# Performance work log

Measured on AMD Instinct MI355X. Metric: run time of the kernel, lower is better.

## Reference

```python
import jax, jax.numpy as jnp
import numpy as np

N_EMBD = 2048
N_EXPERTS = 8
MOE_LOSS_COEFF = 0.01


def setup_inputs() -> dict:
    key = jax.random.key(0)
    kx, kw = jax.random.split(key)
    x = jax.random.normal(kx, (4, 4096, N_EMBD), dtype=jnp.float32)
    # nn.Linear(n_embd, n_experts, bias=False): weight [n_experts, n_embd]
    bound = 1.0 / np.sqrt(N_EMBD)
    W = jax.random.uniform(kw, (N_EXPERTS, N_EMBD), dtype=jnp.float32,
                           minval=-bound, maxval=bound)
    return {"x": x, "W": W}


def reference(x, W):
    n_experts = W.shape[0]
    # gate linear: logits [B, T, E]
    logits = jnp.einsum("btd,ed->bte", x, W)
    probs = jax.nn.softmax(logits, axis=-1)
    # top-2 selection and renormalization
    top2_vals, top2_idx = jax.lax.top_k(probs, 2)  # [B,T,2]
    gate_probs_top2 = top2_vals / jnp.sum(top2_vals, axis=-1, keepdims=True)
    # aux load-balancing loss stats
    importance = jnp.mean(probs, axis=(0, 1))  # [E]
    top1_idx = jnp.argmax(probs, axis=-1)      # [B,T]
    one_hot = jax.nn.one_hot(top1_idx, n_experts, dtype=jnp.float32)
    load = jnp.mean(one_hot, axis=(0, 1))      # [E]
    aux_loss = n_experts * jnp.sum(importance * load) * MOE_LOSS_COEFF
    return gate_probs_top2, top2_idx, aux_loss
```

## Files before the change

### kernel.cpp

```cpp
#include <hip/hip_runtime.h>

#define NEMBD 2048
#define ROW4 (NEMBD / 4)
#define CHUNKS (ROW4 / 64)

__global__ __launch_bounds__(256) void gate_kernel(
    const float* __restrict__ x, const float* __restrict__ W,
    float* __restrict__ out, float* __restrict__ ws, int ntok)
{
    const int tid  = threadIdx.x;
    const int lane = tid & 63;
    const int wid  = tid >> 6;

    const int t0 = blockIdx.x * 8 + wid * 2;
    const bool va0 = t0 < ntok, va1 = (t0 + 1) < ntok;

    const float4* X4 = (const float4*)x;
    const float4* W4 = (const float4*)W;
    float* out_p = out;
    float* out_i = out + 2 * ntok;

    float a[16];
    #pragma unroll
    for (int q = 0; q < 16; ++q) a[q] = 0.f;

    const float4 z4 = make_float4(0.f, 0.f, 0.f, 0.f);

    #pragma unroll 2
    for (int i = 0; i < CHUNKS; ++i) {
        const int col = i * 64 + lane;
        float4 x0 = va0 ? X4[(size_t)t0 * ROW4 + col] : z4;
        float4 x1 = va1 ? X4[(size_t)(t0 + 1) * ROW4 + col] : z4;
        #pragma unroll
        for (int e = 0; e < 8; ++e) {
            float4 wv = W4[e * ROW4 + col];
            a[e]     += x0.x * wv.x + x0.y * wv.y + x0.z * wv.z + x0.w * wv.w;
            a[8 + e] += x1.x * wv.x + x1.y * wv.y + x1.z * wv.z + x1.w * wv.w;
        }
    }

    #pragma unroll
    for (int q = 0; q < 16; ++q) a[q] += __shfl_xor(a[q], 32, 64);
    #pragma unroll
    for (int q = 0; q < 16; ++q) a[q] += __shfl_xor(a[q], 16, 64);
    #pragma unroll
    for (int s = 0; s < 4; ++s) {
        const int hm = 8 >> s;
        const bool hi = (lane & hm) != 0;
        #pragma unroll
        for (int q = 0; q < 8; ++q) {
            if (q < hm) {
                float send = hi ? a[q] : a[q + hm];
                float recv = __shfl_xor(send, hm, 64);
                float keep = hi ? a[q + hm] : a[q];
                a[q] = keep + recv;
            }
        }
    }
    const float logit = a[0];
    const int e = lane & 7;
    const int k = (lane >> 3) & 1;
    const bool tvalid = (t0 + k) < ntok;

    float m = logit;
    #pragma unroll
    for (int mm = 1; mm <= 4; mm <<= 1) m = fmaxf(m, __shfl_xor(m, mm, 64));
    float p = __expf(logit - m);
    float ssum = p;
    #pragma unroll
    for (int mm = 1; mm <= 4; mm <<= 1) ssum += __shfl_xor(ssum, mm, 64);
    const float prob = p / ssum;

    float v1 = prob, v2 = -1.f;
    int   i1 = e,    i2 = -1;
    #pragma unroll
    for (int mm = 1; mm <= 4; mm <<= 1) {
        float b1 = __shfl_xor(v1, mm, 64);
        float b2 = __shfl_xor(v2, mm, 64);
        int  bi1 = __shfl_xor(i1, mm, 64);
        int  bi2 = __shfl_xor(i2, mm, 64);
        bool aw = (v1 > b1) || (v1 == b1 && i1 < bi1);
        float w1 = aw ? v1 : b1;  int wi1 = aw ? i1 : bi1;
        float l1 = aw ? b1 : v1;  int li1 = aw ? bi1 : i1;
        float w2 = aw ? v2 : b2;  int wi2 = aw ? i2 : bi2;
        bool sw = (l1 > w2) || (l1 == w2 && li1 < wi2);
        v1 = w1; i1 = wi1;
        v2 = sw ? l1 : w2;  i2 = sw ? li1 : wi2;
    }

    if (e == 0 && lane < 16 && tvalid) {
        const int t = t0 + k;
        const float denom = v1 + v2;
        out_p[2 * t]     = v1 / denom;
        out_p[2 * t + 1] = v2 / denom;
        out_i[2 * t]     = (float)i1;
        out_i[2 * t + 1] = (float)i2;
    }

    float pc = tvalid ? prob : 0.f;
    float oc = (tvalid && e == i1) ? 1.f : 0.f;
    pc += __shfl_xor(pc, 8, 64);
    oc += __shfl_xor(oc, 8, 64);

    __shared__ float part[4][16];
    if (lane < 8) {
        part[wid][lane]     = pc;
        part[wid][lane + 8] = oc;
    }
    __syncthreads();
    if (tid < 16) {
        atomicAdd(&ws[tid],
                  part[0][tid] + part[1][tid] + part[2][tid] + part[3][tid]);
    }
}

__global__ void finalize_kernel(const float* __restrict__ ws,
                                float* __restrict__ out, int ntok)
{
    if (threadIdx.x == 0) {
        const float inv = 1.f / (float)ntok;
        float aux = 0.f;
        #pragma unroll
        for (int e = 0; e < 8; ++e)
            aux += (ws[e] * inv) * (ws[8 + e] * inv);
        out[4 * ntok] = 8.f * aux * 0.01f;
    }
}

extern "C" void kernel_launch(void* const* d_in, const int* in_sizes, int n_in,
                              void* d_out, int out_size, void* d_ws, size_t ws_size,
                              hipStream_t stream)
{
    const float* x = (const float*)d_in[0];
    const float* W = (const float*)d_in[1];
    const int ntok    = in_sizes[0] / NEMBD;
    const int nblocks = (ntok + 7) / 8;

    hipMemsetAsync(d_ws, 0, 16 * sizeof(float), stream);
    gate_kernel<<<nblocks, 256, 0, stream>>>(
        x, W, (float*)d_out, (float*)d_ws, ntok);
    finalize_kernel<<<1, 64, 0, stream>>>(
        (const float*)d_ws, (float*)d_out, ntok);
}
```

Baseline: 215.0 us.

## Stage gate weights in LDS with 1024-thread blocks and per-block partial stats

Result: no change. 211.4 us (-1.7%).

```diff
diff --git a/kernel.cpp b/kernel.cpp
--- a/kernel.cpp
+++ b/kernel.cpp
@@ -3,20 +3,30 @@
 #define NEMBD 2048
 #define ROW4 (NEMBD / 4)
 #define CHUNKS (ROW4 / 64)
+#define NEXP 8
+#define W4N (NEXP * ROW4)
 
-__global__ __launch_bounds__(256) void gate_kernel(
+__global__ __launch_bounds__(1024) void gate_kernel(
     const float* __restrict__ x, const float* __restrict__ W,
     float* __restrict__ out, float* __restrict__ ws, int ntok)
 {
+    __shared__ float4 Wl[W4N];
+
     const int tid  = threadIdx.x;
     const int lane = tid & 63;
     const int wid  = tid >> 6;
 
-    const int t0 = blockIdx.x * 8 + wid * 2;
+    const float4* X4 = (const float4*)x;
+    const float4* W4 = (const float4*)W;
+
+    #pragma unroll
+    for (int k = 0; k < 4; ++k)
+        Wl[tid + k * 1024] = W4[tid + k * 1024];
+    __syncthreads();
+
+    const int t0 = blockIdx.x * 32 + wid * 2;
     const bool va0 = t0 < ntok, va1 = (t0 + 1) < ntok;
 
-    const float4* X4 = (const float4*)x;
-    const float4* W4 = (const float4*)W;
     float* out_p = out;
     float* out_i = out + 2 * ntok;
 
@@ -33,7 +43,7 @@
         float4 x1 = va1 ? X4[(size_t)(t0 + 1) * ROW4 + col] : z4;
         #pragma unroll
         for (int e = 0; e < 8; ++e) {
-            float4 wv = W4[e * ROW4 + col];
+            float4 wv = Wl[e * ROW4 + col];
             a[e]     += x0.x * wv.x + x0.y * wv.y + x0.z * wv.z + x0.w * wv.w;
             a[8 + e] += x1.x * wv.x + x1.y * wv.y + x1.z * wv.z + x1.w * wv.w;
         }
@@ -102,27 +112,43 @@
     pc += __shfl_xor(pc, 8, 64);
     oc += __shfl_xor(oc, 8, 64);
 
-    __shared__ float part[4][16];
-    if (lane < 8) {
-        part[wid][lane]     = pc;
-        part[wid][lane + 8] = oc;
-    }
+    float* part = (float*)Wl;
+    __syncthreads();
+    if (lane < 8)       part[wid * 16 + lane] = pc;
+    else if (lane < 16) part[wid * 16 + lane] = oc;
     __syncthreads();
     if (tid < 16) {
-        atomicAdd(&ws[tid],
-                  part[0][tid] + part[1][tid] + part[2][tid] + part[3][tid]);
+        float v = 0.f;
+        #pragma unroll
+        for (int w = 0; w < 16; ++w) v += part[w * 16 + tid];
+        ws[blockIdx.x * 16 + tid] = v;
     }
 }
 
 __global__ void finalize_kernel(const float* __restrict__ ws,
-                                float* __restrict__ out, int ntok)
+                                float* __restrict__ out, int nblk, int ntok)
 {
-    if (threadIdx.x == 0) {
+    __shared__ float s[16][16];
+    __shared__ float tot[16];
+    const int t = threadIdx.x;
+    const int slot = t & 15, chunk = t >> 4;
+    float p = 0.f;
+    for (int b = chunk; b < nblk; b += 16) p += ws[b * 16 + slot];
+    s[chunk][slot] = p;
+    __syncthreads();
+    if (t < 16) {
+        float v = 0.f;
+        #pragma unroll
+        for (int c = 0; c < 16; ++c) v += s[c][t];
+        tot[t] = v;
+    }
+    __syncthreads();
+    if (t == 0) {
         const float inv = 1.f / (float)ntok;
         float aux = 0.f;
         #pragma unroll
         for (int e = 0; e < 8; ++e)
-            aux += (ws[e] * inv) * (ws[8 + e] * inv);
+            aux += (tot[e] * inv) * (tot[8 + e] * inv);
         out[4 * ntok] = 8.f * aux * 0.01f;
     }
 }
@@ -134,11 +160,10 @@
     const float* x = (const float*)d_in[0];
     const float* W = (const float*)d_in[1];
     const int ntok    = in_sizes[0] / NEMBD;
-    const int nblocks = (ntok + 7) / 8;
+    const int nblocks = (ntok + 31) / 32;
 
-    hipMemsetAsync(d_ws, 0, 16 * sizeof(float), stream);
-    gate_kernel<<<nblocks, 256, 0, stream>>>(
+    gate_kernel<<<nblocks, 1024, 0, stream>>>(
         x, W, (float*)d_out, (float*)d_ws, ntok);
-    finalize_kernel<<<1, 64, 0, stream>>>(
-        (const float*)d_ws, (float*)d_out, ntok);
+    finalize_kernel<<<1, 256, 0, stream>>>(
+        (const float*)d_ws, (float*)d_out, nblocks, ntok);
 }
```
